# Optimization experiments

Measured on AMD Instinct MI355X. Metric: run time of the kernel, lower is better.

## Reference

```python
import jax, jax.numpy as jnp
import numpy as np

N = 50000      # num_users == num_products (required by the original forward's reuse of edge_index)
E = 800000
F_IN = 128
HID = 256
CLS = 64


def sage_conv(x_src, x_dst, e_src, e_dst, w_l, b_l, w_r, num_dst):
    """PyG SAGEConv (mean aggr, bipartite): lin_l(mean_j x_src[j]) + lin_r(x_dst)."""
    msg = x_src[e_src]                                             # [E, d]
    agg = jax.ops.segment_sum(msg, e_dst, num_segments=num_dst)    # [num_dst, d]
    cnt = jax.ops.segment_sum(jnp.ones((e_dst.shape[0],), x_src.dtype), e_dst,
                              num_segments=num_dst)
    mean = agg / jnp.maximum(cnt, 1.0)[:, None]
    return mean @ w_l.T + b_l + x_dst @ w_r.T


def setup_inputs() -> dict:
    key = jax.random.key(0)
    ks = jax.random.split(key, 16)
    def lin(k, out_d, in_d):
        s = 1.0 / np.sqrt(in_d)
        return jax.random.uniform(k, (out_d, in_d), jnp.float32, -s, s)
    return {
        'x_user': jax.random.normal(ks[0], (N, F_IN), jnp.float32),
        'x_product': jax.random.normal(ks[1], (N, F_IN), jnp.float32),
        'edge_index': jax.random.randint(ks[2], (2, E), 0, N, jnp.int64 if jax.config.jax_enable_x64 else jnp.int32),
        # user_conv1: (F_IN,F_IN)->HID
        'w_u1_l': lin(ks[3], HID, F_IN), 'b_u1': jnp.zeros((HID,), jnp.float32), 'w_u1_r': lin(ks[4], HID, F_IN),
        # product_conv1: (F_IN,F_IN)->HID
        'w_p1_l': lin(ks[5], HID, F_IN), 'b_p1': jnp.zeros((HID,), jnp.float32), 'w_p1_r': lin(ks[6], HID, F_IN),
        # user_conv2: (HID,HID)->CLS
        'w_u2_l': lin(ks[7], CLS, HID), 'b_u2': jnp.zeros((CLS,), jnp.float32), 'w_u2_r': lin(ks[8], CLS, HID),
        # product_conv2: (HID,HID)->CLS
        'w_p2_l': lin(ks[9], CLS, HID), 'b_p2': jnp.zeros((CLS,), jnp.float32), 'w_p2_r': lin(ks[10], CLS, HID),
    }


def reference(x_user, x_product, edge_index,
              w_u1_l, b_u1, w_u1_r, w_p1_l, b_p1, w_p1_r,
              w_u2_l, b_u2, w_u2_r, w_p2_l, b_p2, w_p2_r):
    u_idx, p_idx = edge_index[0], edge_index[1]
    # layer 1 (eval mode: dropout is identity)
    x_user_1 = jax.nn.relu(sage_conv(x_user, x_product, u_idx, p_idx,
                                     w_u1_l, b_u1, w_u1_r, N))        # [N, HID] (dst=product-sized)
    x_product_1 = jax.nn.relu(sage_conv(x_product, x_user, p_idx, u_idx,
                                        w_p1_l, b_p1, w_p1_r, N))     # [N, HID]
    # layer 2 (same edge_index reuse as the original code)
    x_user_2 = sage_conv(x_user_1, x_product_1, u_idx, p_idx,
                         w_u2_l, b_u2, w_u2_r, N)                     # [N, CLS]
    x_product_2 = sage_conv(x_product_1, x_user_1, p_idx, u_idx,
                            w_p2_l, b_p2, w_p2_r, N)                  # [N, CLS]
    return x_user_2, x_product_2
```

## Files before the change

### kernel.cpp

```cpp
#include <hip/hip_runtime.h>
#include <stdint.h>

#define Nn 50000
#define Ee 800000
#define FIN 128
#define HIDD 256
#define CLSS 64

#define NBIN 98
#define BSH 9
#define BINSZ 512
#define BCAP 16384
#define EPB 2048
#define NEB ((Ee + EPB - 1) / EPB)

#define MT_TOT 782
#define GX 112

#define SHP 264

typedef unsigned int uint_t;
typedef unsigned short us_t;
typedef __attribute__((ext_vector_type(8))) short short8;
typedef __attribute__((ext_vector_type(4))) float f32x4;
typedef __attribute__((ext_vector_type(2))) float f32x2;

__device__ inline float bflo(uint_t v) { union { uint_t u; float f; } c; c.u = v << 16; return c.f; }
__device__ inline float bfhi(uint_t v) { union { uint_t u; float f; } c; c.u = v & 0xffff0000u; return c.f; }
__device__ inline us_t f2bf(float f) {
    union { float f; uint_t u; } c; c.f = f;
    uint_t u = c.u;
    u += 0x7fffu + ((u >> 16) & 1u);
    return (us_t)(u >> 16);
}

#define GLOAD(gp, lp)                                                      \
    __builtin_amdgcn_global_load_lds(                                      \
        (const __attribute__((address_space(1))) unsigned int*)(gp),       \
        (__attribute__((address_space(3))) unsigned int*)(lp), 16, 0, 0)

__global__ __launch_bounds__(512) void k_front(
    const int* __restrict__ ei,
    const float* __restrict__ xu, const float* __restrict__ xp,
    const float* __restrict__ w1, const float* __restrict__ w2,
    const float* __restrict__ w3, const float* __restrict__ w4,
    const float* __restrict__ w5, const float* __restrict__ w6,
    const float* __restrict__ w7, const float* __restrict__ w8,
    us_t* __restrict__ cu, us_t* __restrict__ cp,
    uint_t* __restrict__ f8u, uint_t* __restrict__ f8p,
    us_t* __restrict__ wc10, us_t* __restrict__ wc11,
    us_t* __restrict__ wc20, us_t* __restrict__ wc21,
    int* __restrict__ bin_cnt,
    uint_t* __restrict__ ent_p, uint_t* __restrict__ ent_u) {
    __shared__ int hist[2 * NBIN];
    __shared__ int base[2 * NBIN];
    int bx = blockIdx.x, tid = threadIdx.x;

    if (bx < NEB) {
        int e0 = bx * EPB;
        int n = Ee - e0; if (n > EPB) n = EPB;
        for (int i = tid; i < 2 * NBIN; i += 512) hist[i] = 0;
        __syncthreads();
        for (int i = tid; i < n; i += 512) {
            int u = ei[e0 + i], p = ei[Ee + e0 + i];
            atomicAdd(&hist[p >> BSH], 1);
            atomicAdd(&hist[NBIN + (u >> BSH)], 1);
        }
        __syncthreads();
        for (int i = tid; i < 2 * NBIN; i += 512) {
            int c = hist[i];
            base[i] = c ? atomicAdd(&bin_cnt[i], c) : 0;
        }
        __syncthreads();
        for (int i = tid; i < 2 * NBIN; i += 512) hist[i] = base[i];
        __syncthreads();
        for (int i = tid; i < n; i += 512) {
            int u = ei[e0 + i], p = ei[Ee + e0 + i];
            int bp = p >> BSH, bu = u >> BSH;
            int rp = atomicAdd(&hist[bp], 1);
            if (rp < BCAP)
                ent_p[(size_t)bp * BCAP + rp] = ((uint_t)(p & (BINSZ - 1)) << 16) | (uint_t)u;
            int ru = atomicAdd(&hist[NBIN + bu], 1);
            if (ru < BCAP)
                ent_u[(size_t)bu * BCAP + ru] = ((uint_t)(u & (BINSZ - 1)) << 16) | (uint_t)p;
        }
    } else if (bx < NEB + 96) {
        int i = (bx - NEB) * 512 + tid;
        const float* wp; us_t* dst;
        if (i < 32768) {
            int seg = i >> 13; int loc = i & 8191;
            int row = loc >> 5, col = (loc & 31) * 4;
            switch (seg) {
                case 0: wp = w1; dst = wc10 + (size_t)row * 256 + col; break;
                case 1: wp = w2; dst = wc10 + (size_t)row * 256 + 128 + col; break;
                case 2: wp = w3; dst = wc11 + (size_t)row * 256 + col; break;
                default: wp = w4; dst = wc11 + (size_t)row * 256 + 128 + col; break;
            }
            float4 v = reinterpret_cast<const float4*>(wp)[i & 8191];
            ushort4 o;
            o.x = f2bf(v.x); o.y = f2bf(v.y); o.z = f2bf(v.z); o.w = f2bf(v.w);
            *reinterpret_cast<ushort4*>(dst) = o;
        } else {
            int j = i - 32768;
            int seg = j >> 12; int loc = j & 4095;
            switch (seg) {
                case 0: wp = w5; dst = wc20; break;
                case 1: wp = w6; dst = wc21 + 64 * 256; break;
                case 2: wp = w7; dst = wc21; break;
                default: wp = w8; dst = wc20 + 64 * 256; break;
            }
            float4 v = reinterpret_cast<const float4*>(wp)[loc];
            ushort4 o;
            o.x = f2bf(v.x); o.y = f2bf(v.y); o.z = f2bf(v.z); o.w = f2bf(v.w);
            reinterpret_cast<ushort4*>(dst)[loc] = o;
        }
    } else {
        int bcx = bx - NEB - 96;
        int side = bcx & 1;
        const float* in = side ? xp : xu;
        us_t* comb = side ? cu : cp;
        uint_t* o8 = side ? f8p : f8u;
        const int n4 = (Nn * FIN) / 4;
        int i = (bcx >> 1) * 512 + tid;
        int stride = 256 * 512;
        for (; i < n4; i += stride) {
            float4 v = reinterpret_cast<const float4*>(in)[i];
            ushort4 o;
            o.x = f2bf(v.x); o.y = f2bf(v.y); o.z = f2bf(v.z); o.w = f2bf(v.w);
            int node = i >> 5;
            int col = (i & 31) * 4;
            *reinterpret_cast<ushort4*>(comb + (size_t)node * 256 + 128 + col) = o;
            int pk = __builtin_amdgcn_cvt_pk_fp8_f32(v.x, v.y, 0, false);
            pk = __builtin_amdgcn_cvt_pk_fp8_f32(v.z, v.w, pk, true);
            o8[i] = (uint_t)pk;
        }
    }
}

__global__ __launch_bounds__(512) void k_scatter(
    const uint_t* __restrict__ ent_p, const uint_t* __restrict__ ent_u,
    const int* __restrict__ bin_cnt,
    int* __restrict__ off, int* __restrict__ cnt,
    int* __restrict__ src_p, int* __restrict__ src_u) {
    __shared__ int ca[BINSZ];
    __shared__ int cb[BINSZ];
    __shared__ int bb[128];
    int side = blockIdx.y, b = blockIdx.x, t = threadIdx.x;
    const uint_t* E = (side ? ent_u : ent_p) + (size_t)b * BCAP;
    int* src = side ? src_u : src_p;

    if (t < 128) {
        int v = 0;
        if (t < NBIN) { v = bin_cnt[side * NBIN + t]; if (v > BCAP) v = BCAP; }
        bb[t] = v;
    }
    __syncthreads();
    #pragma unroll
    for (int d = 1; d < 128; d <<= 1) {
        int x = 0;
        if (t < 128 && t >= d) x = bb[t - d];
        __syncthreads();
        if (t < 128) bb[t] += x;
        __syncthreads();
    }
    int nb = bin_cnt[side * NBIN + b]; if (nb > BCAP) nb = BCAP;
    int base = bb[b] - nb;

    ca[t] = 0;
    __syncthreads();
    for (int i = t; i < nb; i += 512)
        atomicAdd(&ca[E[i] >> 16], 1);
    __syncthreads();
    int v = ca[t];
    int* A = ca; int* B = cb;
    #pragma unroll
    for (int d = 1; d < BINSZ; d <<= 1) {
        int x = A[t] + ((t >= d) ? A[t - d] : 0);
        B[t] = x;
        __syncthreads();
        int* tmp = A; A = B; B = tmp;
    }
    int excl = A[t] - v;
    B[t] = excl;
    __syncthreads();
    for (int i = t; i < nb; i += 512) {
        uint_t e = E[i];
        int sl = atomicAdd(&B[e >> 16], 1);
        src[base + sl] = (int)(e & 0xffffu);
    }
    int d = (b << BSH) + t;
    if (d < Nn) {
        off[side * Nn + d] = base + excl;
        cnt[side * Nn + d] = v;
    }
}

__global__ __launch_bounds__(256) void k_agg1(
    const uint4* __restrict__ xu8, const uint4* __restrict__ xp8,
    const int* __restrict__ off, const int* __restrict__ cnt,
    const int* __restrict__ src_p, const int* __restrict__ src_u,
    us_t* __restrict__ cu, us_t* __restrict__ cp) {
    int side = blockIdx.y;
    const uint4* X = side ? xp8 : xu8;
    const int* of = off + side * Nn;
    const int* cn = cnt + side * Nn;
    const int* sr = side ? src_u : src_p;
    us_t* out = side ? cp : cu;

    int node = blockIdx.x * 32 + (threadIdx.x >> 3);
    if (node >= Nn) return;
    int l = threadIdx.x & 7;
    int s = of[node], c = cn[node];
    float ac[16];
    #pragma unroll
    for (int i = 0; i < 16; ++i) ac[i] = 0.f;

    int j = 0;
    for (; j + 8 <= c; j += 8) {
        int ss[8];
        #pragma unroll
        for (int q = 0; q < 8; ++q) ss[q] = sr[s + j + q];
        uint4 vv[8];
        #pragma unroll
        for (int q = 0; q < 8; ++q) vv[q] = X[(size_t)ss[q] * 8 + l];
        #pragma unroll
        for (int q = 0; q < 8; ++q) {
            const uint_t* pw = reinterpret_cast<const uint_t*>(&vv[q]);
            #pragma unroll
            for (int h = 0; h < 4; ++h) {
                f32x2 plo = __builtin_amdgcn_cvt_pk_f32_fp8((int)pw[h], false);
                f32x2 phi = __builtin_amdgcn_cvt_pk_f32_fp8((int)pw[h], true);
                ac[h * 4 + 0] += plo[0]; ac[h * 4 + 1] += plo[1];
                ac[h * 4 + 2] += phi[0]; ac[h * 4 + 3] += phi[1];
            }
        }
    }
    for (; j < c; ++j) {
        uint4 v0 = X[(size_t)sr[s + j] * 8 + l];
        const uint_t* pw = reinterpret_cast<const uint_t*>(&v0);
        #pragma unroll
        for (int h = 0; h < 4; ++h) {
            f32x2 plo = __builtin_amdgcn_cvt_pk_f32_fp8((int)pw[h], false);
            f32x2 phi = __builtin_amdgcn_cvt_pk_f32_fp8((int)pw[h], true);
            ac[h * 4 + 0] += plo[0]; ac[h * 4 + 1] += plo[1];
            ac[h * 4 + 2] += phi[0]; ac[h * 4 + 3] += phi[1];
        }
    }
    float inv = 1.0f / fmaxf((float)c, 1.0f);
    uint_t ow[8];
    #pragma unroll
    for (int i = 0; i < 8; ++i)
        ow[i] = (uint_t)f2bf(ac[2 * i] * inv) | ((uint_t)f2bf(ac[2 * i + 1] * inv) << 16);
    uint4* dst = reinterpret_cast<uint4*>(out + (size_t)node * 256 + l * 16);
    uint4 o0 = {ow[0], ow[1], ow[2], ow[3]};
    uint4 o1 = {ow[4], ow[5], ow[6], ow[7]};
    dst[0] = o0;
    dst[1] = o1;
}

__global__ __launch_bounds__(256) void k_agg2(
    const uint4* __restrict__ tu, const uint4* __restrict__ tp,
    const int* __restrict__ off, const int* __restrict__ cnt,
    const int* __restrict__ src_p, const int* __restrict__ src_u,
    float* __restrict__ ou, float* __restrict__ op) {
    int side = blockIdx.y;
    const uint4* T = side ? tp : tu;
    const int* of = off + side * Nn;
    const int* cn = cnt + side * Nn;
    const int* sr = side ? src_u : src_p;
    float* out = side ? op : ou;

    int node = blockIdx.x * 32 + (threadIdx.x >> 3);
    if (node >= Nn) return;
    int l = threadIdx.x & 7;
    int s = of[node], c = cn[node];
    float ac[8];
    #pragma unroll
    for (int i = 0; i < 8; ++i) ac[i] = 0.f;

    int j = 0;
    for (; j + 8 <= c; j += 8) {
        int ss[8];
        #pragma unroll
        for (int q = 0; q < 8; ++q) ss[q] = sr[s + j + q];
        uint4 vv[8];
        #pragma unroll
        for (int q = 0; q < 8; ++q) vv[q] = T[(size_t)ss[q] * 8 + l];
        #pragma unroll
        for (int q = 0; q < 8; ++q) {
            const uint_t* pw = reinterpret_cast<const uint_t*>(&vv[q]);
            #pragma unroll
            for (int h = 0; h < 4; ++h) {
                ac[h * 2 + 0] += bflo(pw[h]);
                ac[h * 2 + 1] += bfhi(pw[h]);
            }
        }
    }
    for (; j < c; ++j) {
        uint4 v0 = T[(size_t)sr[s + j] * 8 + l];
        const uint_t* pw = reinterpret_cast<const uint_t*>(&v0);
        #pragma unroll
        for (int h = 0; h < 4; ++h) {
            ac[h * 2 + 0] += bflo(pw[h]);
            ac[h * 2 + 1] += bfhi(pw[h]);
        }
    }
    float inv = 1.0f / fmaxf((float)c, 1.0f);
    float4* po = reinterpret_cast<float4*>(out + (size_t)node * 64) + l * 2;
    float4 p0 = po[0], p1 = po[1];
    p0.x += ac[0] * inv; p0.y += ac[1] * inv; p0.z += ac[2] * inv; p0.w += ac[3] * inv;
    p1.x += ac[4] * inv; p1.y += ac[5] * inv; p1.z += ac[6] * inv; p1.w += ac[7] * inv;
    po[0] = p0; po[1] = p1;
}

#define STAGE_A(Ag, mt, b)                                                          \
    {                                                                               \
        int base_ = (mt) * 64;                                                      \
        _Pragma("unroll")                                                           \
        for (int ii = 0; ii < 4; ++ii) {                                            \
            int s_ = ii * 512 + tid;                                                \
            int row_ = s_ >> 5, ks_ = s_ & 31;                                      \
            int ksl_ = ks_ ^ (row_ & 7);                                            \
            int gr_ = base_ + row_; if (gr_ >= Nn) gr_ = Nn - 1;                    \
            GLOAD((Ag) + (size_t)gr_ * 256 + ksl_ * 8, &sA[b][(s_ - lane) * 8]);    \
        }                                                                           \
    }

__global__ __launch_bounds__(512) void k_mmf(
    const us_t* __restrict__ cu, const us_t* __restrict__ cp,
    const us_t* __restrict__ wc10, const us_t* __restrict__ wc11,
    const us_t* __restrict__ wc20, const us_t* __restrict__ wc21,
    const float* __restrict__ bu1, const float* __restrict__ bp1,
    const float* __restrict__ bu2, const float* __restrict__ bp2,
    us_t* __restrict__ tu, us_t* __restrict__ tp,
    float* __restrict__ ou, float* __restrict__ op) {
    __shared__ us_t sA[2][64 * 256];
    __shared__ us_t sH[64 * SHP];
    int tid = threadIdx.x, lane = tid & 63;
    int wv = tid >> 6, wr = wv >> 2, wc = wv & 3;
    int job = blockIdx.y;
    const us_t* Ag = job ? cp : cu;
    const us_t* W1 = job ? wc11 : wc10;
    const us_t* W2 = job ? wc21 : wc20;
    const float* b1 = job ? bp1 : bu1;
    const float* b2 = job ? bu2 : bp2;
    us_t* T = job ? tp : tu;
    float* O = job ? ou : op;

    short8 wf1[4][8];
    #pragma unroll
    for (int n = 0; n < 4; ++n)
        #pragma unroll
        for (int ks = 0; ks < 8; ++ks) {
            int col = wc * 64 + n * 16 + (lane & 15);
            wf1[n][ks] = *reinterpret_cast<const short8*>(
                W1 + (size_t)col * 256 + ks * 32 + (lane >> 4) * 8);
        }
    float bv1[4];
    #pragma unroll
    for (int n = 0; n < 4; ++n) bv1[n] = b1[wc * 64 + n * 16 + (lane & 15)];

    short8 wf2[2][8];
    #pragma unroll
    for (int n = 0; n < 2; ++n)
        #pragma unroll
        for (int ks = 0; ks < 8; ++ks) {
            int col = wc * 32 + n * 16 + (lane & 15);
            wf2[n][ks] = *reinterpret_cast<const short8*>(
                W2 + (size_t)col * 256 + ks * 32 + (lane >> 4) * 8);
        }
    float bv2[2];
    #pragma unroll
    for (int n = 0; n < 2; ++n) {
        int col = wc * 32 + n * 16 + (lane & 15);
        bv2[n] = (col >= 64) ? b2[col - 64] : 0.f;
    }

    int bx = blockIdx.x;
    int NT = (MT_TOT - 1 - bx) / GX + 1;
    STAGE_A(Ag, bx, 0);
    for (int t = 0; t < NT; ++t) {
        int mt = bx + t * GX;
        if (t + 1 < NT) {
            STAGE_A(Ag, bx + (t + 1) * GX, (t + 1) & 1);
            asm volatile("s_waitcnt vmcnt(4)" ::: "memory");
        } else {
            asm volatile("s_waitcnt vmcnt(0)" ::: "memory");
        }
        __syncthreads();
        const us_t* sAc = sA[t & 1];

        f32x4 acc1[2][4];
        #pragma unroll
        for (int m = 0; m < 2; ++m)
            #pragma unroll
            for (int n = 0; n < 4; ++n)
                #pragma unroll
                for (int i = 0; i < 4; ++i) acc1[m][n][i] = 0.f;

        #pragma unroll
        for (int ks = 0; ks < 8; ++ks) {
            short8 af[2];
            #pragma unroll
            for (int m = 0; m < 2; ++m) {
                int row = wr * 32 + m * 16 + (lane & 15);
                int sl = (ks * 4 + (lane >> 4)) ^ (row & 7);
                af[m] = *reinterpret_cast<const short8*>(&sAc[row * 256 + sl * 8]);
            }
            #pragma unroll
            for (int m = 0; m < 2; ++m)
                #pragma unroll
                for (int n = 0; n < 4; ++n)
                    acc1[m][n] = __builtin_amdgcn_mfma_f32_16x16x32_bf16(
                        af[m], wf1[n][ks], acc1[m][n], 0, 0, 0);
        }

        #pragma unroll
        for (int n = 0; n < 4; ++n) {
            int col = wc * 64 + n * 16 + (lane & 15);
            #pragma unroll
            for (int m = 0; m < 2; ++m) {
                int r0 = wr * 32 + m * 16 + ((lane >> 4) << 2);
                #pragma unroll
                for (int j = 0; j < 4; ++j)
                    sH[(r0 + j) * SHP + col] =
                        f2bf(fmaxf(acc1[m][n][j] + bv1[n], 0.f));
            }
        }
        __syncthreads();

        f32x4 acc2[2][2];
        #pragma unroll
        for (int m = 0; m < 2; ++m)
            #pragma unroll
            for (int n = 0; n < 2; ++n)
                #pragma unroll
                for (int i = 0; i < 4; ++i) acc2[m][n][i] = 0.f;

        #pragma unroll
        for (int ks = 0; ks < 8; ++ks) {
            short8 af2[2];
            #pragma unroll
            for (int m = 0; m < 2; ++m) {
                int row = wr * 32 + m * 16 + (lane & 15);
                af2[m] = *reinterpret_cast<const short8*>(
                    &sH[row * SHP + ks * 32 + (lane >> 4) * 8]);
            }
            #pragma unroll
            for (int m = 0; m < 2; ++m)
                #pragma unroll
                for (int n = 0; n < 2; ++n)
                    acc2[m][n] = __builtin_amdgcn_mfma_f32_16x16x32_bf16(
                        af2[m], wf2[n][ks], acc2[m][n], 0, 0, 0);
        }

        int mbase = mt * 64;
        #pragma unroll
        for (int n = 0; n < 2; ++n) {
            int col = wc * 32 + n * 16 + (lane & 15);
            bool top = col < 64;
            int cc = top ? col : col - 64;
            #pragma unroll
            for (int m = 0; m < 2; ++m) {
                int row0 = mbase + wr * 32 + m * 16 + ((lane >> 4) << 2);
                #pragma unroll
                for (int j = 0; j < 4; ++j) {
                    int row = row0 + j;
                    if (row >= Nn) continue;
                    float v = acc2[m][n][j] + bv2[n];
                    if (top) T[(size_t)row * 64 + cc] = f2bf(v);
                    else     O[(size_t)row * 64 + cc] = v;
                }
            }
        }
    }
}

extern "C" void kernel_launch(void* const* d_in, const int* in_sizes, int n_in,
                              void* d_out, int out_size, void* d_ws, size_t ws_size,
                              hipStream_t stream) {
    const float* x_user    = (const float*)d_in[0];
    const float* x_product = (const float*)d_in[1];
    const int*   ei        = (const int*)d_in[2];
    const float* w_u1_l = (const float*)d_in[3];
    const float* b_u1   = (const float*)d_in[4];
    const float* w_u1_r = (const float*)d_in[5];
    const float* w_p1_l = (const float*)d_in[6];
    const float* b_p1   = (const float*)d_in[7];
    const float* w_p1_r = (const float*)d_in[8];
    const float* w_u2_l = (const float*)d_in[9];
    const float* b_u2   = (const float*)d_in[10];
    const float* w_u2_r = (const float*)d_in[11];
    const float* w_p2_l = (const float*)d_in[12];
    const float* b_p2   = (const float*)d_in[13];
    const float* w_p2_r = (const float*)d_in[14];

    float* out_u = (float*)d_out;
    float* out_p = out_u + (size_t)Nn * CLSS;

    char* w = (char*)d_ws;
    int* bin_cnt  = (int*)w; w += (size_t)2 * NBIN * 4;
    int* off  = (int*)w;  w += (size_t)2 * Nn * 4;
    int* cnt  = (int*)w;  w += (size_t)2 * Nn * 4;
    int* src_p = (int*)w; w += (size_t)Ee * 4;
    int* src_u = (int*)w; w += (size_t)Ee * 4;
    uint_t* ent_p = (uint_t*)w; w += (size_t)NBIN * BCAP * 4;
    uint_t* ent_u = (uint_t*)w; w += (size_t)NBIN * BCAP * 4;
    uintptr_t a = (uintptr_t)w; a = (a + 255) & ~(uintptr_t)255; w = (char*)a;
    us_t* cu   = (us_t*)w; w += (size_t)Nn * 256 * 2;
    us_t* cp   = (us_t*)w; w += (size_t)Nn * 256 * 2;
    uint_t* xf8u = (uint_t*)w; w += (size_t)Nn * FIN;
    uint_t* xf8p = (uint_t*)w; w += (size_t)Nn * FIN;
    us_t* tbuf_u = (us_t*)w; w += (size_t)Nn * CLSS * 2;
    us_t* tbuf_p = (us_t*)w; w += (size_t)Nn * CLSS * 2;
    us_t* wc10 = (us_t*)w; w += (size_t)256 * 256 * 2;
    us_t* wc11 = (us_t*)w; w += (size_t)256 * 256 * 2;
    us_t* wc20 = (us_t*)w; w += (size_t)128 * 256 * 2;
    us_t* wc21 = (us_t*)w; w += (size_t)128 * 256 * 2;

    hipMemsetAsync(bin_cnt, 0, (size_t)2 * NBIN * 4, stream);
    k_front<<<NEB + 96 + 512, 512, 0, stream>>>(
        ei, x_user, x_product,
        w_u1_l, w_u1_r, w_p1_l, w_p1_r, w_u2_l, w_u2_r, w_p2_l, w_p2_r,
        cu, cp, xf8u, xf8p, wc10, wc11, wc20, wc21,
        bin_cnt, ent_p, ent_u);
    dim3 gsc(NBIN, 2);
    k_scatter<<<gsc, 512, 0, stream>>>(ent_p, ent_u, bin_cnt,
                                       off, cnt, src_p, src_u);

    dim3 ga1((Nn + 31) / 32, 2);
    k_agg1<<<ga1, 256, 0, stream>>>((const uint4*)xf8u, (const uint4*)xf8p,
                                    off, cnt, src_p, src_u, cu, cp);

    dim3 g1(GX, 2);
    k_mmf<<<g1, 512, 0, stream>>>(cu, cp, wc10, wc11, wc20, wc21,
                                  b_u1, b_p1, b_u2, b_p2,
                                  tbuf_u, tbuf_p, out_u, out_p);

    dim3 ga2((Nn + 31) / 32, 2);
    k_agg2<<<ga2, 256, 0, stream>>>((const uint4*)tbuf_u, (const uint4*)tbuf_p,
                                    off, cnt, src_p, src_u, out_u, out_p);
}
```

Measured before the change: 179.8 us.

## Shrink fused MLP row tile to 32 and launch more blocks per CU

The fused two-layer matmul kernel now processes 32-row tiles instead of 64-row tiles. All 8 waves share the same rows and split the output columns, so each wave holds fewer weight fragments and accumulators. The grid grows from 112 to 256 blocks per job, and launch bounds request 4 blocks per CU to raise occupancy and spread work across more CUs. In exchange, each block reuses its weight registers over fewer rows, so per-block weight loads are amortised over less work.

```diff
diff --git a/kernel.cpp b/kernel.cpp
--- a/kernel.cpp
+++ b/kernel.cpp
@@ -14,8 +14,8 @@
 #define EPB 2048
 #define NEB ((Ee + EPB - 1) / EPB)
 
-#define MT_TOT 782
-#define GX 112
+#define MT32 1563
+#define GXF 256
 
 #define SHP 264
 
@@ -313,11 +313,11 @@
     po[0] = p0; po[1] = p1;
 }
 
-#define STAGE_A(Ag, mt, b)                                                          \
+#define STAGE_A32(Ag, mt, b)                                                        \
     {                                                                               \
-        int base_ = (mt) * 64;                                                      \
+        int base_ = (mt) * 32;                                                      \
         _Pragma("unroll")                                                           \
-        for (int ii = 0; ii < 4; ++ii) {                                            \
+        for (int ii = 0; ii < 2; ++ii) {                                            \
             int s_ = ii * 512 + tid;                                                \
             int row_ = s_ >> 5, ks_ = s_ & 31;                                      \
             int ksl_ = ks_ ^ (row_ & 7);                                            \
@@ -326,7 +326,7 @@
         }                                                                           \
     }
 
-__global__ __launch_bounds__(512) void k_mmf(
+__global__ __launch_bounds__(512, 4) void k_mmf(
     const us_t* __restrict__ cu, const us_t* __restrict__ cp,
     const us_t* __restrict__ wc10, const us_t* __restrict__ wc11,
     const us_t* __restrict__ wc20, const us_t* __restrict__ wc21,
@@ -334,10 +334,10 @@
     const float* __restrict__ bu2, const float* __restrict__ bp2,
     us_t* __restrict__ tu, us_t* __restrict__ tp,
     float* __restrict__ ou, float* __restrict__ op) {
-    __shared__ us_t sA[2][64 * 256];
-    __shared__ us_t sH[64 * SHP];
+    __shared__ us_t sA[2][32 * 256];
+    __shared__ us_t sH[32 * SHP];
     int tid = threadIdx.x, lane = tid & 63;
-    int wv = tid >> 6, wr = wv >> 2, wc = wv & 3;
+    int wc = tid >> 6;
     int job = blockIdx.y;
     const us_t* Ag = job ? cp : cu;
     const us_t* W1 = job ? wc11 : wc10;
@@ -347,54 +347,50 @@
     us_t* T = job ? tp : tu;
     float* O = job ? ou : op;
 
-    short8 wf1[4][8];
-    #pragma unroll
-    for (int n = 0; n < 4; ++n)
+    short8 wf1[2][8];
+    #pragma unroll
+    for (int n = 0; n < 2; ++n)
         #pragma unroll
         for (int ks = 0; ks < 8; ++ks) {
-            int col = wc * 64 + n * 16 + (lane & 15);
+            int col = wc * 32 + n * 16 + (lane & 15);
             wf1[n][ks] = *reinterpret_cast<const short8*>(
                 W1 + (size_t)col * 256 + ks * 32 + (lane >> 4) * 8);
         }
-    float bv1[4];
-    #pragma unroll
-    for (int n = 0; n < 4; ++n) bv1[n] = b1[wc * 64 + n * 16 + (lane & 15)];
-
-    short8 wf2[2][8];
-    #pragma unroll
-    for (int n = 0; n < 2; ++n)
-        #pragma unroll
-        for (int ks = 0; ks < 8; ++ks) {
-            int col = wc * 32 + n * 16 + (lane & 15);
-            wf2[n][ks] = *reinterpret_cast<const short8*>(
-                W2 + (size_t)col * 256 + ks * 32 + (lane >> 4) * 8);
-        }
-    float bv2[2];
-    #pragma unroll
-    for (int n = 0; n < 2; ++n) {
-        int col = wc * 32 + n * 16 + (lane & 15);
-        bv2[n] = (col >= 64) ? b2[col - 64] : 0.f;
-    }
+    float bv1[2];
+    #pragma unroll
+    for (int n = 0; n < 2; ++n) bv1[n] = b1[wc * 32 + n * 16 + (lane & 15)];
+
+    short8 wf2[8];
+    #pragma unroll
+    for (int ks = 0; ks < 8; ++ks) {
+        int col = wc * 16 + (lane & 15);
+        wf2[ks] = *reinterpret_cast<const short8*>(
+            W2 + (size_t)col * 256 + ks * 32 + (lane >> 4) * 8);
+    }
+    int col2 = wc * 16 + (lane & 15);
+    float bv2 = (col2 >= 64) ? b2[col2 - 64] : 0.f;
+    bool top2 = col2 < 64;
+    int cc2 = top2 ? col2 : col2 - 64;
 
     int bx = blockIdx.x;
-    int NT = (MT_TOT - 1 - bx) / GX + 1;
-    STAGE_A(Ag, bx, 0);
+    int NT = (MT32 - 1 - bx) / GXF + 1;
+    STAGE_A32(Ag, bx, 0);
     for (int t = 0; t < NT; ++t) {
-        int mt = bx + t * GX;
+        int mt = bx + t * GXF;
         if (t + 1 < NT) {
-            STAGE_A(Ag, bx + (t + 1) * GX, (t + 1) & 1);
-            asm volatile("s_waitcnt vmcnt(4)" ::: "memory");
+            STAGE_A32(Ag, bx + (t + 1) * GXF, (t + 1) & 1);
+            asm volatile("s_waitcnt vmcnt(2)" ::: "memory");
         } else {
             asm volatile("s_waitcnt vmcnt(0)" ::: "memory");
         }
         __syncthreads();
         const us_t* sAc = sA[t & 1];
 
-        f32x4 acc1[2][4];
+        f32x4 acc1[2][2];
         #pragma unroll
         for (int m = 0; m < 2; ++m)
             #pragma unroll
-            for (int n = 0; n < 4; ++n)
+            for (int n = 0; n < 2; ++n)
                 #pragma unroll
                 for (int i = 0; i < 4; ++i) acc1[m][n][i] = 0.f;
 
@@ -403,24 +399,24 @@
             short8 af[2];
             #pragma unroll
             for (int m = 0; m < 2; ++m) {
-                int row = wr * 32 + m * 16 + (lane & 15);
+                int row = m * 16 + (lane & 15);
                 int sl = (ks * 4 + (lane >> 4)) ^ (row & 7);
                 af[m] = *reinterpret_cast<const short8*>(&sAc[row * 256 + sl * 8]);
             }
             #pragma unroll
             for (int m = 0; m < 2; ++m)
                 #pragma unroll
-                for (int n = 0; n < 4; ++n)
+                for (int n = 0; n < 2; ++n)
                     acc1[m][n] = __builtin_amdgcn_mfma_f32_16x16x32_bf16(
                         af[m], wf1[n][ks], acc1[m][n], 0, 0, 0);
         }
 
         #pragma unroll
-        for (int n = 0; n < 4; ++n) {
-            int col = wc * 64 + n * 16 + (lane & 15);
+        for (int n = 0; n < 2; ++n) {
+            int col = wc * 32 + n * 16 + (lane & 15);
             #pragma unroll
             for (int m = 0; m < 2; ++m) {
-                int r0 = wr * 32 + m * 16 + ((lane >> 4) << 2);
+                int r0 = m * 16 + ((lane >> 4) << 2);
                 #pragma unroll
                 for (int j = 0; j < 4; ++j)
                     sH[(r0 + j) * SHP + col] =
@@ -429,48 +425,38 @@
         }
         __syncthreads();
 
-        f32x4 acc2[2][2];
+        f32x4 acc2[2];
         #pragma unroll
         for (int m = 0; m < 2; ++m)
             #pragma unroll
-            for (int n = 0; n < 2; ++n)
-                #pragma unroll
-                for (int i = 0; i < 4; ++i) acc2[m][n][i] = 0.f;
+            for (int i = 0; i < 4; ++i) acc2[m][i] = 0.f;
 
         #pragma unroll
         for (int ks = 0; ks < 8; ++ks) {
             short8 af2[2];
             #pragma unroll
             for (int m = 0; m < 2; ++m) {
-                int row = wr * 32 + m * 16 + (lane & 15);
+                int row = m * 16 + (lane & 15);
                 af2[m] = *reinterpret_cast<const short8*>(
                     &sH[row * SHP + ks * 32 + (lane >> 4) * 8]);
             }
             #pragma unroll
             for (int m = 0; m < 2; ++m)
-                #pragma unroll
-                for (int n = 0; n < 2; ++n)
-                    acc2[m][n] = __builtin_amdgcn_mfma_f32_16x16x32_bf16(
-                        af2[m], wf2[n][ks], acc2[m][n], 0, 0, 0);
-        }
-
-        int mbase = mt * 64;
-        #pragma unroll
-        for (int n = 0; n < 2; ++n) {
-            int col = wc * 32 + n * 16 + (lane & 15);
-            bool top = col < 64;
-            int cc = top ? col : col - 64;
-            #pragma unroll
-            for (int m = 0; m < 2; ++m) {
-                int row0 = mbase + wr * 32 + m * 16 + ((lane >> 4) << 2);
-                #pragma unroll
-                for (int j = 0; j < 4; ++j) {
-                    int row = row0 + j;
-                    if (row >= Nn) continue;
-                    float v = acc2[m][n][j] + bv2[n];
-                    if (top) T[(size_t)row * 64 + cc] = f2bf(v);
-                    else     O[(size_t)row * 64 + cc] = v;
-                }
+                acc2[m] = __builtin_amdgcn_mfma_f32_16x16x32_bf16(
+                    af2[m], wf2[ks], acc2[m], 0, 0, 0);
+        }
+
+        int mbase = mt * 32;
+        #pragma unroll
+        for (int m = 0; m < 2; ++m) {
+            int row0 = mbase + m * 16 + ((lane >> 4) << 2);
+            #pragma unroll
+            for (int j = 0; j < 4; ++j) {
+                int row = row0 + j;
+                if (row >= Nn) continue;
+                float v = acc2[m][j] + bv2;
+                if (top2) T[(size_t)row * 64 + cc2] = f2bf(v);
+                else      O[(size_t)row * 64 + cc2] = v;
             }
         }
     }
@@ -532,7 +518,7 @@
     k_agg1<<<ga1, 256, 0, stream>>>((const uint4*)xf8u, (const uint4*)xf8p,
                                     off, cnt, src_p, src_u, cu, cp);
 
-    dim3 g1(GX, 2);
+    dim3 g1(GXF, 2);
     k_mmf<<<g1, 512, 0, stream>>>(cu, cp, wc10, wc11, wc20, wc21,
                                   b_u1, b_p1, b_u2, b_p2,
                                   tbuf_u, tbuf_p, out_u, out_p);
```

Result: faster. 176.1 us (-2.1%).
